# Kernel optimization log

Hardware: AMD Instinct MI355X
Metric: run time of the kernel (lower is better)

## Reference

```python
import jax, jax.numpy as jnp
import numpy as np

B, C, H, W = 8, 256, 32, 32
N = H * W  # 1024; conv1 maps C -> N channels so all bmms are [B,N,N]


def setup_inputs() -> dict:
    key = jax.random.key(0)
    ks = jax.random.split(key, 11)
    s = 0.02  # weight scale to keep softmax logits in a sane range
    return {
        "x":     jax.random.normal(ks[0], (B, C, H, W), jnp.float32),
        "w1":    jax.random.normal(ks[1], (N, C), jnp.float32) * s,
        "b1":    jax.random.normal(ks[2], (N,), jnp.float32) * s,
        "wq":    jax.random.normal(ks[3], (N, N), jnp.float32) * s,
        "bq":    jax.random.normal(ks[4], (N,), jnp.float32) * s,
        "wv":    jax.random.normal(ks[5], (N, N), jnp.float32) * s,
        "bv":    jax.random.normal(ks[6], (N,), jnp.float32) * s,
        "w2":    jax.random.normal(ks[7], (C, N), jnp.float32) * s,
        "b2":    jax.random.normal(ks[8], (C,), jnp.float32) * s,
        "alpha": jax.random.normal(ks[9], (1,), jnp.float32),
        "beta":  jax.random.normal(ks[10], (1,), jnp.float32),
    }


def reference(x, w1, b1, wq, bq, wv, bv, w2, b2, alpha, beta):
    b, c, h, w = x.shape
    n = h * w
    # 1x1 convs as channel matmuls
    x1 = jnp.einsum('bchw,nc->bnhw', x, w1) + b1[None, :, None, None]  # [B,N,H,W]
    g = (jnp.einsum('bnhw,mn->bmhw', x1, wq) + bq[None, :, None, None]).reshape(b, n, n)
    r = (jnp.einsum('bnhw,mn->bmhw', x1, wv) + bv[None, :, None, None]).reshape(b, n, n)
    xf = x1.reshape(b, n, n)          # m^T in the torch code: [B, N_chan, HW]
    m = xf.transpose(0, 2, 1)         # m: [B, HW, N_chan]
    # spatial attention: z_s = softmax(m^T @ g)
    z_s = jax.nn.softmax(jnp.matmul(xf, g), axis=-1)            # [B,N,N]
    # channel attention: z_c = softmax(g^T @ m)
    z_c = jax.nn.softmax(jnp.matmul(g.transpose(0, 2, 1), m), axis=-1)  # [B,N,N]
    p_s = jnp.matmul(z_s, r)                                    # [B,N,HW]
    p_c = jnp.matmul(z_c, m).transpose(0, 2, 1)                 # [B,N,HW]
    p = (alpha[0] * p_s + beta[0] * p_c).reshape(b, n, h, w)
    out = jnp.einsum('bnhw,cn->bchw', p, w2) + b2[None, :, None, None]
    return out
```

## Files before the change

kernel.cpp:

```cpp
#include <hip/hip_runtime.h>
#include <hip/hip_bf16.h>


typedef __attribute__((ext_vector_type(4))) float f4;
typedef __attribute__((ext_vector_type(8))) short s8;
typedef __attribute__((ext_vector_type(4))) unsigned short us4;
typedef __attribute__((ext_vector_type(8))) unsigned short us8;

__device__ __forceinline__ unsigned short f2bf(float f) {
    __hip_bfloat16 h = __float2bfloat16(f);
    return __builtin_bit_cast(unsigned short, h);
}
__device__ __forceinline__ float bf2f(unsigned short u) {
    unsigned int x = ((unsigned int)u) << 16;
    return __builtin_bit_cast(float, x);
}

#define GAS(p) ((const __attribute__((address_space(1))) unsigned int*)(p))
#define LAS(p) ((__attribute__((address_space(3))) unsigned int*)(p))

__global__ __launch_bounds__(256) void prep(
    const float* __restrict__ w1, const float* __restrict__ wq,
    const float* __restrict__ wv, const float* __restrict__ w2,
    unsigned short* __restrict__ w1b, unsigned short* __restrict__ wqb,
    unsigned short* __restrict__ wvb, unsigned short* __restrict__ w2b,
    const float* __restrict__ bq, const float* __restrict__ bv,
    float* __restrict__ biasqv,
    const float* __restrict__ x, unsigned short* __restrict__ xT)
{
    __shared__ float tl[32][33];
    if (blockIdx.x < 2562) {
        long i = (long)blockIdx.x * 256 + threadIdx.x;
        if (i >= 655360) {
            long j = i - 655360;
            if (j < 512) {
                f4 v = (j < 256) ? ((const f4*)bq)[j] : ((const f4*)bv)[j - 256];
                ((f4*)biasqv)[j] = v;
            }
            return;
        }
        const float* src; unsigned short* dst; long base;
        if (i < 65536)               { src = w1; dst = w1b; base = 0; }
        else if (i < 65536+262144)   { src = wq; dst = wqb; base = 65536; }
        else if (i < 65536+524288)   { src = wv; dst = wvb; base = 65536+262144; }
        else                         { src = w2; dst = w2b; base = 65536+524288; }
        long j = i - base;
        f4 v = ((const f4*)src)[j];
        us4 o;
        #pragma unroll
        for (int k = 0; k < 4; ++k) o[k] = f2bf(v[k]);
        ((us4*)dst)[j] = o;
    } else {
        const int idx = blockIdx.x - 2562;
        const int q0 = (idx & 31) * 32;
        const int c0 = ((idx >> 5) & 7) * 32;
        const int b  = idx >> 8;
        const int tx = threadIdx.x & 31, ty = threadIdx.x >> 5;
        #pragma unroll
        for (int j = 0; j < 4; ++j)
            tl[ty + j*8][tx] = x[((long)(b*256 + c0 + ty + j*8))*1024 + q0 + tx];
        __syncthreads();
        #pragma unroll
        for (int j = 0; j < 4; ++j)
            xT[((long)(b*1024 + q0 + ty + j*8))*256 + c0 + tx] = f2bf(tl[tx][ty + j*8]);
    }
}

template<int BIAS, int SPLIT>
__global__ __launch_bounds__(512, 2) void gemm8p(
    const unsigned short* __restrict__ A0, const unsigned short* __restrict__ Bt0,
    int lda, int ldb,
    void* __restrict__ Cv0, void* __restrict__ Cv1, int ldc,
    const float* __restrict__ bias)
{
    constexpr int NT = 16;
    __shared__ __align__(16) unsigned short As[2][2][8192];
    __shared__ __align__(16) unsigned short Bs[2][2][8192];

    const int gx = gridDim.x, gy = gridDim.y;
    const int nwg = gx * gy;
    int d = blockIdx.x + gx * blockIdx.y;
    int swz = (d & 7) * (nwg >> 3) + (d >> 3);
    const int bx = swz % gx;
    const int by = swz / gx;

    const int m0 = by * 256;
    const int n0 = bx * 256;
    const int t  = threadIdx.x;
    const int w  = t >> 6, l = t & 63;
    const int wr = w >> 2, wc = w & 3;
    const int lr = l & 15, lg = l >> 4;

    const unsigned short* Asrc = A0  + (long)m0 * lda;
    const unsigned short* Bsrc = Bt0 + (long)n0 * ldb;

    const int rl4 = l >> 2;
    const int gsw = ((l & 3) ^ ((l >> 3) & 3)) * 8;
    const int rsw = (lr >> 1) & 3;

    auto stage = [&](const unsigned short* src, int ld_, unsigned short* slot,
                     int sp, int kh) {
        #pragma unroll
        for (int i = 0; i < 2; ++i) {
            const int rb = i*128 + w*16;
            __builtin_amdgcn_global_load_lds(
                GAS(src + (long)(rb + rl4)*ld_ + sp*64 + kh*32 + gsw),
                LAS(slot + rb*32), 16, 0, 0);
        }
    };

    f4 acc[8][4];
    #pragma unroll
    for (int i = 0; i < 8; ++i)
        #pragma unroll
        for (int j = 0; j < 4; ++j) acc[i][j] = (f4){0.f, 0.f, 0.f, 0.f};

    s8 aF[4], bF[4];
    auto rdA = [&](int db, int kh, int mh) {
        #pragma unroll
        for (int m = 0; m < 4; ++m) {
            const int R = wr*128 + mh*64 + m*16 + lr;
            aF[m] = *(const s8*)&As[db][kh][R*32 + ((lg ^ rsw) * 8)];
        }
    };
    auto rdB = [&](int db, int kh) {
        #pragma unroll
        for (int n = 0; n < 4; ++n) {
            const int R = wc*64 + n*16 + lr;
            bF[n] = *(const s8*)&Bs[db][kh][R*32 + ((lg ^ rsw) * 8)];
        }
    };

#define MM8(MH)                                                                  \
    __builtin_amdgcn_s_setprio(1);                                               \
    _Pragma("unroll")                                                            \
    for (int m_ = 0; m_ < 4; ++m_)                                               \
        _Pragma("unroll")                                                        \
        for (int n_ = 0; n_ < 4; ++n_)                                           \
            acc[(MH)*4 + m_][n_] = __builtin_amdgcn_mfma_f32_16x16x32_bf16(      \
                aF[m_], bF[n_], acc[(MH)*4 + m_][n_], 0, 0, 0);                  \
    __builtin_amdgcn_s_setprio(0);

#define PH8(DB, KH, MH, RB, STG, VM)                                             \
    rdA(DB, KH, MH);                                                             \
    if (RB) rdB(DB, KH);                                                         \
    STG;                                                                         \
    __builtin_amdgcn_sched_barrier(0);                                           \
    __builtin_amdgcn_s_barrier();                                                \
    asm volatile("s_waitcnt lgkmcnt(0)" ::: "memory");                           \
    __builtin_amdgcn_sched_barrier(0);                                           \
    MM8(MH);                                                                     \
    VM;                                                                          \
    __builtin_amdgcn_s_barrier();

    stage(Asrc, lda, &As[0][0][0], 0, 0);
    stage(Bsrc, ldb, &Bs[0][0][0], 0, 0);
    stage(Asrc, lda, &As[0][1][0], 0, 1);
    stage(Bsrc, ldb, &Bs[0][1][0], 0, 1);
    stage(Asrc, lda, &As[1][0][0], 1, 0);
    stage(Bsrc, ldb, &Bs[1][0][0], 1, 0);
    asm volatile("s_waitcnt vmcnt(4)" ::: "memory");
    __builtin_amdgcn_sched_barrier(0);
    __builtin_amdgcn_s_barrier();

    for (int j = 0; j < NT/2; ++j) {
        const int tb = 2*j + 1;
        const int t2 = (2*j + 2) & (NT - 1);
        const int t3 = (2*j + 3) & (NT - 1);
        PH8(0,0,0, 1, stage(Asrc, lda, &As[1][1][0], tb, 1), (void)0)
        PH8(0,0,1, 0, stage(Bsrc, ldb, &Bs[1][1][0], tb, 1), (void)0)
        PH8(0,1,0, 1, stage(Asrc, lda, &As[0][0][0], t2, 0), (void)0)
        PH8(0,1,1, 0, stage(Bsrc, ldb, &Bs[0][0][0], t2, 0),
            asm volatile("s_waitcnt vmcnt(4)" ::: "memory"))
        PH8(1,0,0, 1, stage(Asrc, lda, &As[0][1][0], t2, 1), (void)0)
        PH8(1,0,1, 0, stage(Bsrc, ldb, &Bs[0][1][0], t2, 1), (void)0)
        PH8(1,1,0, 1, stage(Asrc, lda, &As[1][0][0], t3, 0), (void)0)
        PH8(1,1,1, 0, stage(Bsrc, ldb, &Bs[1][0][0], t3, 0),
            asm volatile("s_waitcnt vmcnt(4)" ::: "memory"))
    }
#undef PH8
#undef MM8

    void* Cd = Cv0; int nbase = n0;
    if (SPLIT && n0 >= 1024) { Cd = Cv1; nbase = n0 - 1024; }

    const int rbase = lg * 4;
    #pragma unroll
    for (int mi = 0; mi < 8; ++mi) {
        #pragma unroll
        for (int n = 0; n < 4; ++n) {
            const int row  = m0 + wr*128 + mi*16 + rbase;
            const int col  = nbase + wc*64 + n*16 + lr;
            const int bcol = n0    + wc*64 + n*16 + lr;
            #pragma unroll
            for (int j = 0; j < 4; ++j) {
                float v = acc[mi][n][j];
                if (BIAS == 2) v += bias[bcol];
                ((unsigned short*)Cd)[(long)(row + j)*ldc + col] = f2bf(v);
            }
        }
    }
}

template<int BIAS, int OUTF32, int STATS>
__global__ __launch_bounds__(512, 2) void gemm256(
    const unsigned short* __restrict__ A0, const unsigned short* __restrict__ Bt0,
    long sA, long sB, int lda, int ldb,
    void* __restrict__ Cv0, long sC, int ldc,
    const float* __restrict__ bias, int nt1,
    float* __restrict__ csp, float* __restrict__ rsp)
{
    __shared__ __align__(16) unsigned short As[3][16384];
    __shared__ __align__(16) unsigned short Bs[3][8192];

    const int gx = gridDim.x, gy = gridDim.y;
    const int nwg = gx * gy * gridDim.z;
    int d = blockIdx.x + gx * (blockIdx.y + gy * blockIdx.z);
    int swz = (d & 7) * (nwg >> 3) + (d >> 3);
    const int bx = swz % gx; int tq = swz / gx;
    const int by = tq % gy;  const int bz = tq / gy;

    const int b  = bz;
    const int m0 = by * 256;
    const int n0 = bx * 128;
    const int t  = threadIdx.x;
    const int w  = t >> 6, l = t & 63;
    const int wr = w >> 1, wc = w & 1;
    const int lr = l & 15, lg = l >> 4;

    const unsigned short* A0b = A0  + (long)b * sA;
    const unsigned short* B0b = Bt0 + (long)b * sB;

    const int rl  = l >> 3;
    const int gsw = ((l & 7) ^ (rl & 7)) * 8;

    const int NT = nt1;

    auto stageA = [&](int sp, int bf) {
        const int kt = sp * 64;
        #pragma unroll
        for (int i = 0; i < 4; ++i) {
            const int rb = w*32 + i*8;
            __builtin_amdgcn_global_load_lds(GAS(A0b + (long)(m0 + rb + rl)*lda + kt + gsw),
                                             LAS(&As[bf][rb*64]), 16, 0, 0);
        }
    };
    auto stageB = [&](int sp, int bf) {
        const int kt = sp * 64;
        #pragma unroll
        for (int i = 0; i < 2; ++i) {
            const int rb = w*16 + i*8;
            __builtin_amdgcn_global_load_lds(GAS(B0b + (long)(n0 + rb + rl)*ldb + kt + gsw),
                                             LAS(&Bs[bf][rb*64]), 16, 0, 0);
        }
    };

    f4 acc[4][4];
    #pragma unroll
    for (int i = 0; i < 4; ++i)
        #pragma unroll
        for (int j = 0; j < 4; ++j) acc[i][j] = (f4){0.f, 0.f, 0.f, 0.f};

    stageA(0, 0); stageB(0, 0);
    stageA(1, 1); stageB(1, 1);
    asm volatile("s_waitcnt vmcnt(6)" ::: "memory");
    __builtin_amdgcn_sched_barrier(0);
    __builtin_amdgcn_s_barrier();

    s8 a0[4], b0[4], a1f[4], b1f[4];

    #pragma unroll
    for (int m = 0; m < 4; ++m) {
        const int R = wr*64 + m*16 + lr;
        a0[m] = *(const s8*)&As[0][R*64 + ((lg ^ (R & 7)) * 8)];
    }
    #pragma unroll
    for (int n = 0; n < 4; ++n) {
        const int R = wc*64 + n*16 + lr;
        b0[n] = *(const s8*)&Bs[0][R*64 + ((lg ^ (R & 7)) * 8)];
    }
    asm volatile("s_waitcnt lgkmcnt(0)" ::: "memory");
    __builtin_amdgcn_sched_barrier(0);

    int buf = 0;
    for (int s = 0; s < NT; ++s) {
        int bn = buf + 2; if (bn >= 3) bn -= 3;
        int bx1 = buf + 1; if (bx1 >= 3) bx1 -= 3;

        #pragma unroll
        for (int m = 0; m < 4; ++m) {
            const int R = wr*64 + m*16 + lr;
            a1f[m] = *(const s8*)&As[buf][R*64 + (((4 + lg) ^ (R & 7)) * 8)];
        }
        #pragma unroll
        for (int n = 0; n < 4; ++n) {
            const int R = wc*64 + n*16 + lr;
            b1f[n] = *(const s8*)&Bs[buf][R*64 + (((4 + lg) ^ (R & 7)) * 8)];
        }
        if (s + 2 < NT) stageA(s + 2, bn);
        __builtin_amdgcn_s_setprio(1);
        #pragma unroll
        for (int m = 0; m < 4; ++m)
            #pragma unroll
            for (int n = 0; n < 4; ++n)
                acc[m][n] = __builtin_amdgcn_mfma_f32_16x16x32_bf16(a0[m], b0[n], acc[m][n], 0, 0, 0);
        __builtin_amdgcn_s_setprio(0);
        asm volatile("s_waitcnt lgkmcnt(0)" ::: "memory");
        __builtin_amdgcn_sched_barrier(0);

        if (s + 1 < NT) {
            if (s + 2 < NT) asm volatile("s_waitcnt vmcnt(4)" ::: "memory");
            else            asm volatile("s_waitcnt vmcnt(0)" ::: "memory");
            __builtin_amdgcn_sched_barrier(0);
            __builtin_amdgcn_s_barrier();
            #pragma unroll
            for (int m = 0; m < 4; ++m) {
                const int R = wr*64 + m*16 + lr;
                a0[m] = *(const s8*)&As[bx1][R*64 + ((lg ^ (R & 7)) * 8)];
            }
            #pragma unroll
            for (int n = 0; n < 4; ++n) {
                const int R = wc*64 + n*16 + lr;
                b0[n] = *(const s8*)&Bs[bx1][R*64 + ((lg ^ (R & 7)) * 8)];
            }
            if (s + 2 < NT) stageB(s + 2, bn);
            __builtin_amdgcn_s_setprio(1);
            #pragma unroll
            for (int m = 0; m < 4; ++m)
                #pragma unroll
                for (int n = 0; n < 4; ++n)
                    acc[m][n] = __builtin_amdgcn_mfma_f32_16x16x32_bf16(a1f[m], b1f[n], acc[m][n], 0, 0, 0);
            __builtin_amdgcn_s_setprio(0);
            asm volatile("s_waitcnt lgkmcnt(0)" ::: "memory");
            __builtin_amdgcn_sched_barrier(0);
        } else {
            __builtin_amdgcn_s_setprio(1);
            #pragma unroll
            for (int m = 0; m < 4; ++m)
                #pragma unroll
                for (int n = 0; n < 4; ++n)
                    acc[m][n] = __builtin_amdgcn_mfma_f32_16x16x32_bf16(a1f[m], b1f[n], acc[m][n], 0, 0, 0);
            __builtin_amdgcn_s_setprio(0);
        }

        buf = bx1;
    }

    const int rbase = lg * 4;
    float csum[4] = {0.f, 0.f, 0.f, 0.f};
    float rsum[16];
    #pragma unroll
    for (int i = 0; i < 16; ++i) rsum[i] = 0.f;

    #pragma unroll
    for (int m = 0; m < 4; ++m) {
        #pragma unroll
        for (int n = 0; n < 4; ++n) {
            const int row  = m0 + wr*64 + m*16 + rbase;
            const int col  = n0 + wc*64 + n*16 + lr;
            #pragma unroll
            for (int j = 0; j < 4; ++j) {
                float v = acc[m][n][j];
                if (BIAS == 1) v += bias[row + j];
                else if (BIAS == 2) v += bias[col];
                const long idx = (long)b*sC + (long)(row + j)*ldc + col;
                if (STATS) {
                    float ev = __expf(v);
                    unsigned short bv = f2bf(ev);
                    ((unsigned short*)Cv0)[idx] = bv;
                    float evr = bf2f(bv);
                    csum[n] += evr;
                    rsum[m*4 + j] += evr;
                } else if (OUTF32) {
                    ((float*)Cv0)[idx] = v;
                } else {
                    ((unsigned short*)Cv0)[idx] = f2bf(v);
                }
            }
        }
    }

    if (STATS) {
        const int p = by*16 + wr*4 + lg;
        #pragma unroll
        for (int n = 0; n < 4; ++n) {
            const int col = n0 + wc*64 + n*16 + lr;
            csp[(long)p*8192 + b*1024 + col] = csum[n];
        }
        const int p2 = bx*32 + wc*16 + lr;
        #pragma unroll
        for (int m = 0; m < 4; ++m)
            #pragma unroll
            for (int j = 0; j < 4; ++j) {
                const int row = m0 + wr*64 + m*16 + rbase + j;
                rsp[(long)(b*1024 + row)*256 + p2] = rsum[m*4 + j];
            }
    }
}

__global__ __launch_bounds__(512, 2) void gemm_dual2(
    const unsigned short* __restrict__ A0, const unsigned short* __restrict__ Bt0,
    const unsigned short* __restrict__ A1, const unsigned short* __restrict__ Bt1,
    const float* __restrict__ rs, const float* __restrict__ cs,
    const float* __restrict__ alpha_p, const float* __restrict__ beta_p,
    unsigned short* __restrict__ C)
{
    constexpr int NT = 32;
    __shared__ __align__(16) unsigned short As[3][16384];
    __shared__ __align__(16) unsigned short Bs[3][8192];

    const int gx = gridDim.x, gy = gridDim.y;
    const int nwg = gx * gy * gridDim.z;
    int d = blockIdx.x + gx * (blockIdx.y + gy * blockIdx.z);
    int swz = (d & 7) * (nwg >> 3) + (d >> 3);
    const int bx = swz % gx; int tq = swz / gx;
    const int by = tq % gy;  const int bz = tq / gy;

    const int b  = bz;
    const int m0 = by * 256;
    const int n0 = bx * 128;
    const int t  = threadIdx.x;
    const int w  = t >> 6, l = t & 63;
    const int wr = w >> 1, wc = w & 1;
    const int lr = l & 15, lg = l >> 4;

    const unsigned short* A0b = A0  + (long)b * 1048576;
    const unsigned short* B0b = Bt0 + (long)b * 1048576;
    const unsigned short* A1b = A1  + (long)b * 1048576;
    const unsigned short* B1b = Bt1 + (long)b * 1048576;

    const int rl  = l >> 3;
    const int gsw = ((l & 7) ^ (rl & 7)) * 8;

    auto stageA = [&](int sp, int bf) {
        const unsigned short* Ap = (sp >= 16) ? A1b : A0b;
        const int kt = ((sp >= 16) ? sp - 16 : sp) * 64;
        #pragma unroll
        for (int i = 0; i < 4; ++i) {
            const int rb = w*32 + i*8;
            __builtin_amdgcn_global_load_lds(GAS(Ap + (long)(m0 + rb + rl)*1024 + kt + gsw),
                                             LAS(&As[bf][rb*64]), 16, 0, 0);
        }
    };
    auto stageB = [&](int sp, int bf) {
        const unsigned short* Bp = (sp >= 16) ? B1b : B0b;
        const int kt = ((sp >= 16) ? sp - 16 : sp) * 64;
        #pragma unroll
        for (int i = 0; i < 2; ++i) {
            const int rb = w*16 + i*8;
            __builtin_amdgcn_global_load_lds(GAS(Bp + (long)(n0 + rb + rl)*1024 + kt + gsw),
                                             LAS(&Bs[bf][rb*64]), 16, 0, 0);
        }
    };

    f4 acc1[4][4], acc2[4][4];
    #pragma unroll
    for (int i = 0; i < 4; ++i)
        #pragma unroll
        for (int j = 0; j < 4; ++j) {
            acc1[i][j] = (f4){0.f, 0.f, 0.f, 0.f};
            acc2[i][j] = (f4){0.f, 0.f, 0.f, 0.f};
        }

    stageA(0, 0); stageB(0, 0);
    stageA(1, 1); stageB(1, 1);
    asm volatile("s_waitcnt vmcnt(6)" ::: "memory");
    __builtin_amdgcn_sched_barrier(0);
    __builtin_amdgcn_s_barrier();

    s8 a0[4], b0[4], a1f[4], b1f[4];

    #pragma unroll
    for (int m = 0; m < 4; ++m) {
        const int R = wr*64 + m*16 + lr;
        a0[m] = *(const s8*)&As[0][R*64 + ((lg ^ (R & 7)) * 8)];
    }
    #pragma unroll
    for (int n = 0; n < 4; ++n) {
        const int R = wc*64 + n*16 + lr;
        b0[n] = *(const s8*)&Bs[0][R*64 + ((lg ^ (R & 7)) * 8)];
    }
    asm volatile("s_waitcnt lgkmcnt(0)" ::: "memory");
    __builtin_amdgcn_sched_barrier(0);

#define DUAL_BODY(ACC)                                                            \
    {                                                                             \
        int bn = buf + 2; if (bn >= 3) bn -= 3;                                   \
        int bx1 = buf + 1; if (bx1 >= 3) bx1 -= 3;                                \
        _Pragma("unroll")                                                         \
        for (int m = 0; m < 4; ++m) {                                             \
            const int R = wr*64 + m*16 + lr;                                      \
            a1f[m] = *(const s8*)&As[buf][R*64 + (((4 + lg) ^ (R & 7)) * 8)];     \
        }                                                                         \
        _Pragma("unroll")                                                         \
        for (int n = 0; n < 4; ++n) {                                             \
            const int R = wc*64 + n*16 + lr;                                      \
            b1f[n] = *(const s8*)&Bs[buf][R*64 + (((4 + lg) ^ (R & 7)) * 8)];     \
        }                                                                         \
        if (s + 2 < NT) stageA(s + 2, bn);                                        \
        __builtin_amdgcn_s_setprio(1);                                            \
        _Pragma("unroll")                                                         \
        for (int m = 0; m < 4; ++m)                                               \
            _Pragma("unroll")                                                     \
            for (int n = 0; n < 4; ++n)                                           \
                ACC[m][n] = __builtin_amdgcn_mfma_f32_16x16x32_bf16(a0[m], b0[n], ACC[m][n], 0, 0, 0); \
        __builtin_amdgcn_s_setprio(0);                                            \
        asm volatile("s_waitcnt lgkmcnt(0)" ::: "memory");                        \
        __builtin_amdgcn_sched_barrier(0);                                        \
        if (s + 1 < NT) {                                                         \
            if (s + 2 < NT) asm volatile("s_waitcnt vmcnt(4)" ::: "memory");      \
            else            asm volatile("s_waitcnt vmcnt(0)" ::: "memory");      \
            __builtin_amdgcn_sched_barrier(0);                                    \
            __builtin_amdgcn_s_barrier();                                         \
            _Pragma("unroll")                                                     \
            for (int m = 0; m < 4; ++m) {                                         \
                const int R = wr*64 + m*16 + lr;                                  \
                a0[m] = *(const s8*)&As[bx1][R*64 + ((lg ^ (R & 7)) * 8)];        \
            }                                                                     \
            _Pragma("unroll")                                                     \
            for (int n = 0; n < 4; ++n) {                                         \
                const int R = wc*64 + n*16 + lr;                                  \
                b0[n] = *(const s8*)&Bs[bx1][R*64 + ((lg ^ (R & 7)) * 8)];        \
            }                                                                     \
            if (s + 2 < NT) stageB(s + 2, bn);                                    \
            __builtin_amdgcn_s_setprio(1);                                        \
            _Pragma("unroll")                                                     \
            for (int m = 0; m < 4; ++m)                                           \
                _Pragma("unroll")                                                 \
                for (int n = 0; n < 4; ++n)                                       \
                    ACC[m][n] = __builtin_amdgcn_mfma_f32_16x16x32_bf16(a1f[m], b1f[n], ACC[m][n], 0, 0, 0); \
            __builtin_amdgcn_s_setprio(0);                                        \
            asm volatile("s_waitcnt lgkmcnt(0)" ::: "memory");                    \
            __builtin_amdgcn_sched_barrier(0);                                    \
        } else {                                                                  \
            __builtin_amdgcn_s_setprio(1);                                        \
            _Pragma("unroll")                                                     \
            for (int m = 0; m < 4; ++m)                                           \
                _Pragma("unroll")                                                 \
                for (int n = 0; n < 4; ++n)                                       \
                    ACC[m][n] = __builtin_amdgcn_mfma_f32_16x16x32_bf16(a1f[m], b1f[n], ACC[m][n], 0, 0, 0); \
            __builtin_amdgcn_s_setprio(0);                                        \
        }                                                                         \
        buf = bx1;                                                                \
    }

    int buf = 0;
    for (int s = 0; s < 16; ++s) DUAL_BODY(acc1)
    for (int s = 16; s < NT; ++s) DUAL_BODY(acc2)
#undef DUAL_BODY

    const float al = alpha_p[0], be = beta_p[0];
    const int rbase = lg * 4;
    float rscv[4];
    #pragma unroll
    for (int n = 0; n < 4; ++n)
        rscv[n] = al / rs[b*1024 + n0 + wc*64 + n*16 + lr];

    #pragma unroll
    for (int m = 0; m < 4; ++m) {
        #pragma unroll
        for (int j = 0; j < 4; ++j) {
            const int row = m0 + wr*64 + m*16 + rbase + j;
            const float csc = be / cs[b*1024 + row];
            #pragma unroll
            for (int n = 0; n < 4; ++n) {
                const int col = n0 + wc*64 + n*16 + lr;
                float v = acc1[m][n][j]*rscv[n] + acc2[m][n][j]*csc;
                C[(long)b*1048576 + (long)row*1024 + col] = f2bf(v);
            }
        }
    }
}

template<int BIAS, int OUTF32, int NT1, int NBUF>
__global__ __launch_bounds__(256) void gemm_pipe(
    const unsigned short* __restrict__ A0, const unsigned short* __restrict__ Bt0,
    long sA, long sB, int lda, int ldb,
    void* __restrict__ Cv0, long sC, int ldc,
    const float* __restrict__ bias)
{
    constexpr int NT = NT1;
    __shared__ __align__(16) unsigned short As[NBUF][4096];
    __shared__ __align__(16) unsigned short Bs[NBUF][4096];

    const int gx = gridDim.x, gy = gridDim.y;
    const int nwg = gx * gy * gridDim.z;
    int d = blockIdx.x + gx * (blockIdx.y + gy * blockIdx.z);
    int swz = (d & 7) * (nwg >> 3) + (d >> 3);
    const int bx = swz % gx; int tq = swz / gx;
    const int by = tq % gy;  const int bz = tq / gy;

    const int b  = bz;
    const int m0 = by * 128;
    const int n0 = bx * 128;
    const int t  = threadIdx.x;
    const int w  = t >> 6, l = t & 63;
    const int wr = w >> 1, wc = w & 1;
    const int lr = l & 15;

    const unsigned short* A0b = A0  + (long)b * sA;
    const unsigned short* B0b = Bt0 + (long)b * sB;

    const int rA   = w*32 + (l >> 2);
    const int cswz = ((l & 3) ^ ((l >> 3) & 3)) * 8;
    const int swzr = (((l >> 4) ^ ((lr >> 1) & 3)) * 8);

    f4 acc[4][4];
    #pragma unroll
    for (int i = 0; i < 4; ++i)
        #pragma unroll
        for (int j = 0; j < 4; ++j) acc[i][j] = (f4){0.f, 0.f, 0.f, 0.f};

    auto stage = [&](int sp, int bf) {
        const int kt = sp * 32;
        __builtin_amdgcn_global_load_lds(GAS(A0b + (long)(m0 + rA     )*lda + kt + cswz), LAS(&As[bf][w*1024      ]), 16, 0, 0);
        __builtin_amdgcn_global_load_lds(GAS(A0b + (long)(m0 + rA + 16)*lda + kt + cswz), LAS(&As[bf][w*1024 + 512]), 16, 0, 0);
        __builtin_amdgcn_global_load_lds(GAS(B0b + (long)(n0 + rA     )*ldb + kt + cswz), LAS(&Bs[bf][w*1024      ]), 16, 0, 0);
        __builtin_amdgcn_global_load_lds(GAS(B0b + (long)(n0 + rA + 16)*ldb + kt + cswz), LAS(&Bs[bf][w*1024 + 512]), 16, 0, 0);
    };

    #pragma unroll
    for (int dpl = 0; dpl < NBUF - 1; ++dpl) stage(dpl, dpl);

    int buf = 0;
    for (int s = 0; s < NT; ++s) {
        if (NBUF >= 4 && s + 2 < NT) asm volatile("s_waitcnt vmcnt(8)" ::: "memory");
        else if (s + 1 < NT)         asm volatile("s_waitcnt vmcnt(4)" ::: "memory");
        else                         asm volatile("s_waitcnt vmcnt(0)" ::: "memory");
        __builtin_amdgcn_s_barrier();
        __builtin_amdgcn_sched_barrier(0);

        s8 aF[4], bF[4];
        #pragma unroll
        for (int m = 0; m < 4; ++m) aF[m] = *(const s8*)&As[buf][(wr*64 + m*16 + lr)*32 + swzr];
        #pragma unroll
        for (int n = 0; n < 4; ++n) bF[n] = *(const s8*)&Bs[buf][(wc*64 + n*16 + lr)*32 + swzr];

        if (s + NBUF - 1 < NT) {
            int bn = buf + NBUF - 1; if (bn >= NBUF) bn -= NBUF;
            stage(s + NBUF - 1, bn);
        }

        __builtin_amdgcn_s_setprio(1);
        #pragma unroll
        for (int m = 0; m < 4; ++m)
            #pragma unroll
            for (int n = 0; n < 4; ++n)
                acc[m][n] = __builtin_amdgcn_mfma_f32_16x16x32_bf16(aF[m], bF[n], acc[m][n], 0, 0, 0);
        __builtin_amdgcn_s_setprio(0);

        if (++buf == NBUF) buf = 0;
    }

    const int rbase = (l >> 4) * 4;
    #pragma unroll
    for (int m = 0; m < 4; ++m) {
        #pragma unroll
        for (int n = 0; n < 4; ++n) {
            const int row = m0 + wr*64 + m*16 + rbase;
            const int col = n0 + wc*64 + n*16 + lr;
            #pragma unroll
            for (int j = 0; j < 4; ++j) {
                float v = acc[m][n][j];
                if (BIAS == 1) v += bias[row + j];
                else if (BIAS == 2) v += bias[col];
                const long idx = (long)b*sC + (long)(row + j)*ldc + col;
                if (OUTF32) ((float*)Cv0)[idx] = v;
                else ((unsigned short*)Cv0)[idx] = f2bf(v);
            }
        }
    }
}

__global__ __launch_bounds__(256) void stats_reduce(
    const float* __restrict__ csp, const float* __restrict__ rsp,
    float* __restrict__ cs, float* __restrict__ rs)
{
    if (blockIdx.x < 32) {
        const int q = blockIdx.x * 256 + threadIdx.x;
        float s = 0.f;
        #pragma unroll
        for (int p = 0; p < 64; ++p) s += csp[(long)p*8192 + q];
        cs[q] = s;
    } else {
        const int blk = blockIdx.x - 32;
        const int w = threadIdx.x >> 6, l = threadIdx.x & 63;
        #pragma unroll
        for (int i = 0; i < 4; ++i) {
            const int row = blk*16 + w*4 + i;
            f4 v = *(const f4*)&rsp[(long)row*256 + l*4];
            float s = v[0] + v[1] + v[2] + v[3];
            #pragma unroll
            for (int off = 32; off; off >>= 1) s += __shfl_xor(s, off);
            if (l == 0) rs[row] = s;
        }
    }
}

__global__ __launch_bounds__(256) void et_trans(
    const unsigned short* __restrict__ E, unsigned short* __restrict__ Et)
{
    __shared__ unsigned short tile[64][65];
    const int b  = blockIdx.z;
    const int i0 = blockIdx.x * 64;
    const int q0 = blockIdx.y * 64;
    const int t  = threadIdx.x;
    const int ch = t & 7, r = t >> 3;
    const unsigned short* Eb = E + (long)b * 1048576;
    #pragma unroll
    for (int pp = 0; pp < 2; ++pp) {
        const int rr = r + pp*32;
        us8 v = *(const us8*)&Eb[(long)(i0 + rr)*1024 + q0 + ch*8];
        #pragma unroll
        for (int e = 0; e < 8; ++e) tile[rr][ch*8 + e] = v[e];
    }
    __syncthreads();
    unsigned short* Etb = Et + (long)b * 1048576;
    #pragma unroll
    for (int pp = 0; pp < 2; ++pp) {
        const int qr = r + pp*32;
        us8 o;
        #pragma unroll
        for (int e = 0; e < 8; ++e) o[e] = tile[ch*8 + e][qr];
        *(us8*)&Etb[(long)(q0 + qr)*1024 + i0 + ch*8] = o;
    }
}

extern "C" void kernel_launch(void* const* d_in, const int* in_sizes, int n_in,
                              void* d_out, int out_size, void* d_ws, size_t ws_size,
                              hipStream_t stream)
{
    const float* x     = (const float*)d_in[0];
    const float* w1    = (const float*)d_in[1];
    const float* b1    = (const float*)d_in[2];
    const float* wq    = (const float*)d_in[3];
    const float* bq    = (const float*)d_in[4];
    const float* wv    = (const float*)d_in[5];
    const float* bv    = (const float*)d_in[6];
    const float* w2    = (const float*)d_in[7];
    const float* b2    = (const float*)d_in[8];
    const float* alpha = (const float*)d_in[9];
    const float* beta  = (const float*)d_in[10];
    float* out = (float*)d_out;

    char* ws = (char*)d_ws;
    size_t off = 0;
    auto alloc = [&](size_t bytes) -> void* {
        void* p = ws + off; off += (bytes + 255) & ~(size_t)255; return p;
    };
    unsigned short* w1b   = (unsigned short*)alloc(1024L*256*2);
    unsigned short* wqvb  = (unsigned short*)alloc(2048L*1024*2);
    unsigned short* w2b   = (unsigned short*)alloc(256L*1024*2);
    float*          biasqv= (float*)alloc(2048L*4);
    float*          cspv  = (float*)alloc(64L*8192*4);
    float*          rspv  = (float*)alloc(8192L*256*4);
    float*          csv   = (float*)alloc(8L*1024*4);
    float*          rsv   = (float*)alloc(8L*1024*4);
    unsigned short* xTb   = (unsigned short*)alloc(8L*1024*256*2);
    unsigned short* x1b   = (unsigned short*)alloc(8L*1024*1024*2);
    unsigned short* x1tb  = (unsigned short*)alloc(8L*1024*1024*2);
    unsigned short* gtb   = (unsigned short*)alloc(8L*1024*1024*2);
    unsigned short* rtb   = (unsigned short*)alloc(8L*1024*1024*2);
    unsigned short* Ptb   = (unsigned short*)alloc(8L*1024*1024*2);
    unsigned short* Eb  = x1tb;
    unsigned short* Etb = gtb;

    const long S1M = 1048576;

    prep<<<4610, 256, 0, stream>>>(w1, wq, wv, w2, w1b, wqvb, wqvb + S1M, w2b,
                                   bq, bv, biasqv, x, xTb);

    gemm256<1,0,0><<<dim3(8, 4, 8), 512, 0, stream>>>(
        w1b, xTb, 0, 262144, 256, 256, x1b, S1M, 1024, b1, 4, nullptr, nullptr);
    gemm256<2,0,0><<<dim3(8, 32, 1), 512, 0, stream>>>(
        xTb, w1b, 0, 0, 256, 256, x1tb, 0, 1024, b1, 4, nullptr, nullptr);
    gemm8p<2,1><<<dim3(8, 32), 512, 0, stream>>>(
        x1tb, wqvb, 1024, 1024, gtb, rtb, 1024, biasqv);
    gemm256<0,0,1><<<dim3(8, 4, 8), 512, 0, stream>>>(
        x1b, gtb, S1M, S1M, 1024, 1024, Eb, S1M, 1024, nullptr, 16, cspv, rspv);
    stats_reduce<<<544, 256, 0, stream>>>(cspv, rspv, csv, rsv);
    et_trans<<<dim3(16, 16, 8), 256, 0, stream>>>(Eb, Etb);
    gemm_dual2<<<dim3(8, 4, 8), 512, 0, stream>>>(
        rtb, Eb, Etb, x1b, rsv, csv, alpha, beta, Ptb);
    gemm_pipe<1,1,32,4><<<dim3(8, 2, 8), 256, 0, stream>>>(
        w2b, Ptb, 0, S1M, 1024, 1024, out, 262144, 1024, b2);
}
```

Baseline: 160.6 us.

## Fuse E transpose into stats GEMM epilogue and merge x1 GEMMs

```diff
diff --git a/kernel.cpp b/kernel.cpp
--- a/kernel.cpp
+++ b/kernel.cpp
@@ -208,7 +208,8 @@
     long sA, long sB, int lda, int ldb,
     void* __restrict__ Cv0, long sC, int ldc,
     const float* __restrict__ bias, int nt1,
-    float* __restrict__ csp, float* __restrict__ rsp)
+    float* __restrict__ csp, float* __restrict__ rsp,
+    unsigned short* __restrict__ Et)
 {
     __shared__ __align__(16) unsigned short As[3][16384];
     __shared__ __align__(16) unsigned short Bs[3][8192];
@@ -347,54 +348,242 @@
     }
 
     const int rbase = lg * 4;
-    float csum[4] = {0.f, 0.f, 0.f, 0.f};
-    float rsum[16];
-    #pragma unroll
-    for (int i = 0; i < 16; ++i) rsum[i] = 0.f;
-
-    #pragma unroll
-    for (int m = 0; m < 4; ++m) {
-        #pragma unroll
-        for (int n = 0; n < 4; ++n) {
-            const int row  = m0 + wr*64 + m*16 + rbase;
-            const int col  = n0 + wc*64 + n*16 + lr;
-            #pragma unroll
-            for (int j = 0; j < 4; ++j) {
-                float v = acc[m][n][j];
-                if (BIAS == 1) v += bias[row + j];
-                else if (BIAS == 2) v += bias[col];
-                const long idx = (long)b*sC + (long)(row + j)*ldc + col;
-                if (STATS) {
-                    float ev = __expf(v);
+
+    if (STATS) {
+        float csum[4] = {0.f, 0.f, 0.f, 0.f};
+        float rsum[16];
+        #pragma unroll
+        for (int i = 0; i < 16; ++i) rsum[i] = 0.f;
+
+        #pragma unroll
+        for (int m = 0; m < 4; ++m) {
+            #pragma unroll
+            for (int n = 0; n < 4; ++n) {
+                const int row = m0 + wr*64 + m*16 + rbase;
+                const int col = n0 + wc*64 + n*16 + lr;
+                us4 eo;
+                #pragma unroll
+                for (int j = 0; j < 4; ++j) {
+                    float ev = __expf(acc[m][n][j]);
                     unsigned short bv = f2bf(ev);
-                    ((unsigned short*)Cv0)[idx] = bv;
+                    ((unsigned short*)Cv0)[(long)b*sC + (long)(row + j)*ldc + col] = bv;
+                    eo[j] = bv;
                     float evr = bf2f(bv);
                     csum[n] += evr;
                     rsum[m*4 + j] += evr;
-                } else if (OUTF32) {
-                    ((float*)Cv0)[idx] = v;
-                } else {
-                    ((unsigned short*)Cv0)[idx] = f2bf(v);
                 }
-            }
-        }
-    }
-
-    if (STATS) {
+                *(us4*)&Et[(long)b*1048576 + (long)col*1024 + row] = eo;
+            }
+        }
+
         const int p = by*16 + wr*4 + lg;
         #pragma unroll
         for (int n = 0; n < 4; ++n) {
             const int col = n0 + wc*64 + n*16 + lr;
             csp[(long)p*8192 + b*1024 + col] = csum[n];
         }
-        const int p2 = bx*32 + wc*16 + lr;
+        #pragma unroll
+        for (int i = 0; i < 16; ++i) {
+            #pragma unroll
+            for (int off = 1; off < 16; off <<= 1)
+                rsum[i] += __shfl_xor(rsum[i], off);
+        }
+        if (lr == 0) {
+            const int p2 = bx*2 + wc;
+            #pragma unroll
+            for (int m = 0; m < 4; ++m)
+                #pragma unroll
+                for (int j = 0; j < 4; ++j) {
+                    const int row = m0 + wr*64 + m*16 + rbase + j;
+                    rsp[(long)(b*1024 + row)*16 + p2] = rsum[m*4 + j];
+                }
+        }
+    } else {
+        #pragma unroll
+        for (int m = 0; m < 4; ++m) {
+            #pragma unroll
+            for (int n = 0; n < 4; ++n) {
+                const int row = m0 + wr*64 + m*16 + rbase;
+                const int col = n0 + wc*64 + n*16 + lr;
+                #pragma unroll
+                for (int j = 0; j < 4; ++j) {
+                    float v = acc[m][n][j];
+                    if (BIAS == 1) v += bias[row + j];
+                    else if (BIAS == 2) v += bias[col];
+                    const long idx = (long)b*sC + (long)(row + j)*ldc + col;
+                    if (OUTF32) ((float*)Cv0)[idx] = v;
+                    else ((unsigned short*)Cv0)[idx] = f2bf(v);
+                }
+            }
+        }
+    }
+}
+
+__global__ __launch_bounds__(512, 2) void gemm_x1(
+    const unsigned short* __restrict__ w1b, const unsigned short* __restrict__ xTb,
+    unsigned short* __restrict__ x1, unsigned short* __restrict__ x1T,
+    const float* __restrict__ b1)
+{
+    constexpr int NT = 4;
+    __shared__ __align__(16) unsigned short As[3][16384];
+    __shared__ __align__(16) unsigned short Bs[3][8192];
+
+    const int gx = gridDim.x, gy = gridDim.y;
+    const int nwg = gx * gy * gridDim.z;
+    int d = blockIdx.x + gx * (blockIdx.y + gy * blockIdx.z);
+    int swz = (d & 7) * (nwg >> 3) + (d >> 3);
+    const int bx = swz % gx; int tq = swz / gx;
+    const int by = tq % gy;  const int bz = tq / gy;
+
+    const bool roleA = (by < 4);
+    const unsigned short* Ap;
+    const unsigned short* Bp;
+    unsigned short* Cp;
+    int m0;
+    if (roleA) {
+        Ap = w1b;
+        Bp = xTb + (long)bz * 262144;
+        Cp = x1  + (long)bz * 1048576;
+        m0 = by * 256;
+    } else {
+        Ap = xTb;
+        Bp = w1b;
+        Cp = x1T;
+        m0 = (bz * 4 + (by - 4)) * 256;
+    }
+    const int n0 = bx * 128;
+    const int t  = threadIdx.x;
+    const int w  = t >> 6, l = t & 63;
+    const int wr = w >> 1, wc = w & 1;
+    const int lr = l & 15, lg = l >> 4;
+
+    const int rl  = l >> 3;
+    const int gsw = ((l & 7) ^ (rl & 7)) * 8;
+
+    auto stageA = [&](int sp, int bf) {
+        const int kt = sp * 64;
+        #pragma unroll
+        for (int i = 0; i < 4; ++i) {
+            const int rb = w*32 + i*8;
+            __builtin_amdgcn_global_load_lds(GAS(Ap + (long)(m0 + rb + rl)*256 + kt + gsw),
+                                             LAS(&As[bf][rb*64]), 16, 0, 0);
+        }
+    };
+    auto stageB = [&](int sp, int bf) {
+        const int kt = sp * 64;
+        #pragma unroll
+        for (int i = 0; i < 2; ++i) {
+            const int rb = w*16 + i*8;
+            __builtin_amdgcn_global_load_lds(GAS(Bp + (long)(n0 + rb + rl)*256 + kt + gsw),
+                                             LAS(&Bs[bf][rb*64]), 16, 0, 0);
+        }
+    };
+
+    f4 acc[4][4];
+    #pragma unroll
+    for (int i = 0; i < 4; ++i)
+        #pragma unroll
+        for (int j = 0; j < 4; ++j) acc[i][j] = (f4){0.f, 0.f, 0.f, 0.f};
+
+    stageA(0, 0); stageB(0, 0);
+    stageA(1, 1); stageB(1, 1);
+    asm volatile("s_waitcnt vmcnt(6)" ::: "memory");
+    __builtin_amdgcn_sched_barrier(0);
+    __builtin_amdgcn_s_barrier();
+
+    s8 a0[4], b0[4], a1f[4], b1f[4];
+
+    #pragma unroll
+    for (int m = 0; m < 4; ++m) {
+        const int R = wr*64 + m*16 + lr;
+        a0[m] = *(const s8*)&As[0][R*64 + ((lg ^ (R & 7)) * 8)];
+    }
+    #pragma unroll
+    for (int n = 0; n < 4; ++n) {
+        const int R = wc*64 + n*16 + lr;
+        b0[n] = *(const s8*)&Bs[0][R*64 + ((lg ^ (R & 7)) * 8)];
+    }
+    asm volatile("s_waitcnt lgkmcnt(0)" ::: "memory");
+    __builtin_amdgcn_sched_barrier(0);
+
+    int buf = 0;
+    for (int s = 0; s < NT; ++s) {
+        int bn = buf + 2; if (bn >= 3) bn -= 3;
+        int bx1 = buf + 1; if (bx1 >= 3) bx1 -= 3;
+
+        #pragma unroll
+        for (int m = 0; m < 4; ++m) {
+            const int R = wr*64 + m*16 + lr;
+            a1f[m] = *(const s8*)&As[buf][R*64 + (((4 + lg) ^ (R & 7)) * 8)];
+        }
+        #pragma unroll
+        for (int n = 0; n < 4; ++n) {
+            const int R = wc*64 + n*16 + lr;
+            b1f[n] = *(const s8*)&Bs[buf][R*64 + (((4 + lg) ^ (R & 7)) * 8)];
+        }
+        if (s + 2 < NT) stageA(s + 2, bn);
+        __builtin_amdgcn_s_setprio(1);
         #pragma unroll
         for (int m = 0; m < 4; ++m)
             #pragma unroll
+            for (int n = 0; n < 4; ++n)
+                acc[m][n] = __builtin_amdgcn_mfma_f32_16x16x32_bf16(a0[m], b0[n], acc[m][n], 0, 0, 0);
+        __builtin_amdgcn_s_setprio(0);
+        asm volatile("s_waitcnt lgkmcnt(0)" ::: "memory");
+        __builtin_amdgcn_sched_barrier(0);
+
+        if (s + 1 < NT) {
+            if (s + 2 < NT) asm volatile("s_waitcnt vmcnt(4)" ::: "memory");
+            else            asm volatile("s_waitcnt vmcnt(0)" ::: "memory");
+            __builtin_amdgcn_sched_barrier(0);
+            __builtin_amdgcn_s_barrier();
+            #pragma unroll
+            for (int m = 0; m < 4; ++m) {
+                const int R = wr*64 + m*16 + lr;
+                a0[m] = *(const s8*)&As[bx1][R*64 + ((lg ^ (R & 7)) * 8)];
+            }
+            #pragma unroll
+            for (int n = 0; n < 4; ++n) {
+                const int R = wc*64 + n*16 + lr;
+                b0[n] = *(const s8*)&Bs[bx1][R*64 + ((lg ^ (R & 7)) * 8)];
+            }
+            if (s + 2 < NT) stageB(s + 2, bn);
+            __builtin_amdgcn_s_setprio(1);
+            #pragma unroll
+            for (int m = 0; m < 4; ++m)
+                #pragma unroll
+                for (int n = 0; n < 4; ++n)
+                    acc[m][n] = __builtin_amdgcn_mfma_f32_16x16x32_bf16(a1f[m], b1f[n], acc[m][n], 0, 0, 0);
+            __builtin_amdgcn_s_setprio(0);
+            asm volatile("s_waitcnt lgkmcnt(0)" ::: "memory");
+            __builtin_amdgcn_sched_barrier(0);
+        } else {
+            __builtin_amdgcn_s_setprio(1);
+            #pragma unroll
+            for (int m = 0; m < 4; ++m)
+                #pragma unroll
+                for (int n = 0; n < 4; ++n)
+                    acc[m][n] = __builtin_amdgcn_mfma_f32_16x16x32_bf16(a1f[m], b1f[n], acc[m][n], 0, 0, 0);
+            __builtin_amdgcn_s_setprio(0);
+        }
+
+        buf = bx1;
+    }
+
+    const int rbase = lg * 4;
+    #pragma unroll
+    for (int m = 0; m < 4; ++m) {
+        #pragma unroll
+        for (int n = 0; n < 4; ++n) {
+            const int row = m0 + wr*64 + m*16 + rbase;
+            const int col = n0 + wc*64 + n*16 + lr;
+            const float cb = roleA ? 0.f : b1[col];
+            #pragma unroll
             for (int j = 0; j < 4; ++j) {
-                const int row = m0 + wr*64 + m*16 + rbase + j;
-                rsp[(long)(b*1024 + row)*256 + p2] = rsum[m*4 + j];
-            }
+                float v = acc[m][n][j] + (roleA ? b1[(row + j) & 1023] : cb);
+                Cp[(long)(row + j)*1024 + col] = f2bf(v);
+            }
+        }
     }
 }
 
@@ -683,46 +872,14 @@
         for (int p = 0; p < 64; ++p) s += csp[(long)p*8192 + q];
         cs[q] = s;
     } else {
-        const int blk = blockIdx.x - 32;
-        const int w = threadIdx.x >> 6, l = threadIdx.x & 63;
+        const int row = (blockIdx.x - 32) * 256 + threadIdx.x;
+        float s = 0.f;
         #pragma unroll
         for (int i = 0; i < 4; ++i) {
-            const int row = blk*16 + w*4 + i;
-            f4 v = *(const f4*)&rsp[(long)row*256 + l*4];
-            float s = v[0] + v[1] + v[2] + v[3];
-            #pragma unroll
-            for (int off = 32; off; off >>= 1) s += __shfl_xor(s, off);
-            if (l == 0) rs[row] = s;
-        }
-    }
-}
-
-__global__ __launch_bounds__(256) void et_trans(
-    const unsigned short* __restrict__ E, unsigned short* __restrict__ Et)
-{
-    __shared__ unsigned short tile[64][65];
-    const int b  = blockIdx.z;
-    const int i0 = blockIdx.x * 64;
-    const int q0 = blockIdx.y * 64;
-    const int t  = threadIdx.x;
-    const int ch = t & 7, r = t >> 3;
-    const unsigned short* Eb = E + (long)b * 1048576;
-    #pragma unroll
-    for (int pp = 0; pp < 2; ++pp) {
-        const int rr = r + pp*32;
-        us8 v = *(const us8*)&Eb[(long)(i0 + rr)*1024 + q0 + ch*8];
-        #pragma unroll
-        for (int e = 0; e < 8; ++e) tile[rr][ch*8 + e] = v[e];
-    }
-    __syncthreads();
-    unsigned short* Etb = Et + (long)b * 1048576;
-    #pragma unroll
-    for (int pp = 0; pp < 2; ++pp) {
-        const int qr = r + pp*32;
-        us8 o;
-        #pragma unroll
-        for (int e = 0; e < 8; ++e) o[e] = tile[ch*8 + e][qr];
-        *(us8*)&Etb[(long)(q0 + qr)*1024 + i0 + ch*8] = o;
+            f4 v = *(const f4*)&rsp[(long)row*16 + i*4];
+            s += v[0] + v[1] + v[2] + v[3];
+        }
+        rs[row] = s;
     }
 }
 
@@ -753,7 +910,7 @@
     unsigned short* w2b   = (unsigned short*)alloc(256L*1024*2);
     float*          biasqv= (float*)alloc(2048L*4);
     float*          cspv  = (float*)alloc(64L*8192*4);
-    float*          rspv  = (float*)alloc(8192L*256*4);
+    float*          rspv  = (float*)alloc(8192L*16*4);
     float*          csv   = (float*)alloc(8L*1024*4);
     float*          rsv   = (float*)alloc(8L*1024*4);
     unsigned short* xTb   = (unsigned short*)alloc(8L*1024*256*2);
@@ -761,25 +918,21 @@
     unsigned short* x1tb  = (unsigned short*)alloc(8L*1024*1024*2);
     unsigned short* gtb   = (unsigned short*)alloc(8L*1024*1024*2);
     unsigned short* rtb   = (unsigned short*)alloc(8L*1024*1024*2);
+    unsigned short* Etb   = (unsigned short*)alloc(8L*1024*1024*2);
     unsigned short* Ptb   = (unsigned short*)alloc(8L*1024*1024*2);
     unsigned short* Eb  = x1tb;
-    unsigned short* Etb = gtb;
 
     const long S1M = 1048576;
 
     prep<<<4610, 256, 0, stream>>>(w1, wq, wv, w2, w1b, wqvb, wqvb + S1M, w2b,
                                    bq, bv, biasqv, x, xTb);
 
-    gemm256<1,0,0><<<dim3(8, 4, 8), 512, 0, stream>>>(
-        w1b, xTb, 0, 262144, 256, 256, x1b, S1M, 1024, b1, 4, nullptr, nullptr);
-    gemm256<2,0,0><<<dim3(8, 32, 1), 512, 0, stream>>>(
-        xTb, w1b, 0, 0, 256, 256, x1tb, 0, 1024, b1, 4, nullptr, nullptr);
+    gemm_x1<<<dim3(8, 8, 8), 512, 0, stream>>>(w1b, xTb, x1b, x1tb, b1);
     gemm8p<2,1><<<dim3(8, 32), 512, 0, stream>>>(
         x1tb, wqvb, 1024, 1024, gtb, rtb, 1024, biasqv);
     gemm256<0,0,1><<<dim3(8, 4, 8), 512, 0, stream>>>(
-        x1b, gtb, S1M, S1M, 1024, 1024, Eb, S1M, 1024, nullptr, 16, cspv, rspv);
-    stats_reduce<<<544, 256, 0, stream>>>(cspv, rspv, csv, rsv);
-    et_trans<<<dim3(16, 16, 8), 256, 0, stream>>>(Eb, Etb);
+        x1b, gtb, S1M, S1M, 1024, 1024, Eb, S1M, 1024, nullptr, 16, cspv, rspv, Etb);
+    stats_reduce<<<64, 256, 0, stream>>>(cspv, rspv, csv, rsv);
     gemm_dual2<<<dim3(8, 4, 8), 512, 0, stream>>>(
         rtb, Eb, Etb, x1b, rsv, csv, alpha, beta, Ptb);
     gemm_pipe<1,1,32,4><<<dim3(8, 2, 8), 256, 0, stream>>>(
```

Result: slower. 165.9 us (+3.3%).
